# Kernel tuning notes

Measured on AMD Instinct MI355X. Metric: run time of the kernel, lower is better.

## Reference

```python
import jax, jax.numpy as jnp
import numpy as np

B, T, H, HEADS, K, L = 64, 512, 512, 4, 3, 16
R, A = 256, 9


def _pe(t, h):
    pos = np.arange(t)[:, None].astype(np.float32)
    div = np.exp(-np.log(10000.0) * np.arange(0, h, 2).astype(np.float32) / h)
    pe = np.zeros((t, h), np.float32)
    pe[:, 0::2] = np.sin(pos * div)
    pe[:, 1::2] = np.cos(pos * div)
    return jnp.asarray(pe)


def _ln(x, g, b, eps=1e-5):
    m = x.mean(-1, keepdims=True)
    v = ((x - m) ** 2).mean(-1, keepdims=True)
    return (x - m) * jax.lax.rsqrt(v + eps) * g + b


def _dwconv(x, k):
    # x [B,T,C], k [K,C]: depthwise temporal conv, SAME padding
    kern = k[:, None, :]  # [K, 1, C] in WIO layout, groups = C
    return jax.lax.conv_general_dilated(
        x, kern, (1,), 'SAME',
        dimension_numbers=('NWC', 'WIO', 'NWC'),
        feature_group_count=x.shape[-1])


def setup_inputs():
    key = jax.random.key(0)
    ks = jax.random.split(key, 16)
    n = lambda i, shape, s=0.02: jax.random.normal(ks[i], shape, jnp.float32) * s
    return dict(
        rssi=jax.random.normal(ks[0], (B, T, R), jnp.float32),
        accl=jax.random.normal(ks[1], (B, T, A), jnp.float32),
        rssi_W=n(2, (R, H)), rssi_b=jnp.zeros((H,), jnp.float32),
        accl_W=n(3, (A, H)), accl_b=jnp.zeros((H,), jnp.float32),
        conv_r=n(4, (K, H), 0.1), conv_a=n(5, (K, H), 0.1),
        Wq=n(6, (H, H)), Wk=n(7, (H, H)), Wv=n(8, (H, H)), Wo=n(9, (H, H)),
        ln1_g=jnp.ones((H,), jnp.float32), ln1_b=jnp.zeros((H,), jnp.float32),
        W1=n(10, (H, 4 * H)), b1=jnp.zeros((4 * H,), jnp.float32),
        W2=n(11, (4 * H, H)), b2=jnp.zeros((H,), jnp.float32),
        ln2_g=jnp.ones((H,), jnp.float32), ln2_b=jnp.zeros((H,), jnp.float32),
        loc_W=n(12, (H, L)), loc_b=jnp.zeros((L,), jnp.float32),
        start_trans=n(13, (L,), 0.1), end_trans=n(14, (L,), 0.1),
        trans=n(15, (L, L), 0.1),
    )


def _emissions(rssi, accl, rssi_W, rssi_b, accl_W, accl_b, conv_r, conv_a,
               Wq, Wk, Wv, Wo, ln1_g, ln1_b, W1, b1, W2, b2, ln2_g, ln2_b,
               loc_W, loc_b):
    t, h = rssi.shape[1], rssi_W.shape[1]
    pe = _pe(t, h)
    r = rssi @ rssi_W + rssi_b + pe                   # [B,T,H]
    a = accl @ accl_W + accl_b + pe                   # [B,T,H]
    x = _dwconv(r, conv_r) + _dwconv(a, conv_a)       # dual-conv fusion
    b_, t_, _ = x.shape
    dh = h // HEADS
    q = (x @ Wq).reshape(b_, t_, HEADS, dh)
    k = (x @ Wk).reshape(b_, t_, HEADS, dh)
    v = (x @ Wv).reshape(b_, t_, HEADS, dh)
    logits = jnp.einsum('bqhd,bkhd->bhqk', q, k) / jnp.sqrt(jnp.float32(dh))
    attn = jax.nn.softmax(logits, axis=-1)
    o = jnp.einsum('bhqk,bkhd->bqhd', attn, v).reshape(b_, t_, h) @ Wo
    x = _ln(x + o, ln1_g, ln1_b)
    f = jax.nn.relu(x @ W1 + b1) @ W2 + b2
    x = _ln(x + f, ln2_g, ln2_b)
    return x @ loc_W + loc_b                          # emissions [B,T,L]


def _viterbi(em, start_trans, end_trans, trans):
    # torchcrf-style Viterbi decode (batch_first, full-length sequences)
    score0 = start_trans + em[:, 0]                   # [B,L]

    def step(score, em_t):
        tot = score[:, :, None] + trans[None] + em_t[:, None, :]  # [B,L,L]
        return tot.max(axis=1), tot.argmax(axis=1)

    score, hist = jax.lax.scan(step, score0, jnp.swapaxes(em[:, 1:], 0, 1))
    final = score + end_trans
    last = jnp.argmax(final, axis=-1)                 # [B]
    best = jnp.max(final, axis=-1)                    # [B] best-path score

    def back(tag, h):
        prev = jnp.take_along_axis(h, tag[:, None], axis=1)[:, 0]
        return prev, prev

    _, path = jax.lax.scan(back, last, hist, reverse=True)
    tags = jnp.concatenate([path, last[None]], axis=0)  # [T,B]
    return jnp.swapaxes(tags, 0, 1).astype(jnp.int64), best


def reference(rssi, accl, rssi_W, rssi_b, accl_W, accl_b, conv_r, conv_a,
              Wq, Wk, Wv, Wo, ln1_g, ln1_b, W1, b1, W2, b2, ln2_g, ln2_b,
              loc_W, loc_b, start_trans, end_trans, trans):
    em = _emissions(rssi, accl, rssi_W, rssi_b, accl_W, accl_b, conv_r, conv_a,
                    Wq, Wk, Wv, Wo, ln1_g, ln1_b, W1, b1, W2, b2,
                    ln2_g, ln2_b, loc_W, loc_b)
    tags, _ = _viterbi(em, start_trans, end_trans, trans)
    return tags  # [B,T] int decoded locations
```

## Files before the change

kernel.cpp:

```cpp
#include <hip/hip_runtime.h>
#include <math.h>

constexpr int Bc = 64, Tc = 512, Hc = 512, HEADSc = 4, Lc = 16, Rc = 256, Ac = 9;
constexpr int DH = 128;

#define F_BIAS 1
#define F_PE   2
#define F_ADDC 4
#define F_RELU 8
#define F_DIV  16
#define F_QKV  32

using short8   = __attribute__((ext_vector_type(8)))  short;
using floatx16 = __attribute__((ext_vector_type(16))) float;
using ushort4v = __attribute__((ext_vector_type(4)))  unsigned short;

struct S3 { unsigned short h, m, l; };
__device__ inline S3 split3(float v)
{
    S3 r;
    unsigned u = __float_as_uint(v);
    r.h = (unsigned short)(u >> 16);
    float r1 = v - __uint_as_float(u & 0xffff0000u);
    unsigned u1 = __float_as_uint(r1);
    r.m = (unsigned short)(u1 >> 16);
    float r2 = r1 - __uint_as_float(u1 & 0xffff0000u);
    r.l = (unsigned short)(__float_as_uint(r2) >> 16);
    return r;
}

template<bool ASP, bool BSP>
__global__ __launch_bounds__(256)
void mgemm(const float* __restrict__ Af, const unsigned short* __restrict__ Asp,
           long long aPS,
           const float* __restrict__ Bf, const unsigned short* __restrict__ Bsp,
           long long bPS,
           float* __restrict__ C, const float* __restrict__ bias,
           const float* __restrict__ pe,
           int M, int N, int K, int lda, int ldb, int ldc,
           long long s1A, long long s2A, long long s1B, long long s2B,
           long long s1C, long long s2C, float divv, int flags)
{
    int z = blockIdx.z, z1 = z >> 2, z2 = z & 3;
    if (ASP) Asp += (size_t)z1 * s1A + (size_t)z2 * s2A;
    else     Af  += (size_t)z1 * s1A + (size_t)z2 * s2A;
    if (BSP) Bsp += (size_t)z1 * s1B + (size_t)z2 * s2B;
    else     Bf  += (size_t)z1 * s1B + (size_t)z2 * s2B;
    if (!(flags & F_QKV)) C += (size_t)z1 * s1C + (size_t)z2 * s2C;

    __shared__ unsigned short As[3][128][34];
    __shared__ unsigned short Bs[3][128][34];

    int bm = blockIdx.y * 128, bn = blockIdx.x * 128;
    int tid = threadIdx.x;
    int lane = tid & 63, wave = tid >> 6;
    int wr = wave >> 1, wc = wave & 1;
    int l31 = lane & 31, khalf = lane >> 5;

    floatx16 acc[2][2];
    #pragma unroll
    for (int i = 0; i < 2; i++)
        #pragma unroll
        for (int j = 0; j < 2; j++)
            #pragma unroll
            for (int e = 0; e < 16; e++) acc[i][j][e] = 0.f;

    for (int k0 = 0; k0 < K; k0 += 32) {
        if (ASP) {
            #pragma unroll
            for (int it = 0; it < 2; it++) {
                int s = tid + 256 * it;
                int rr = s >> 2, kc = (s & 3) << 3;
                size_t ga = (size_t)(bm + rr) * lda + k0 + kc;
                *(short8*)&As[0][rr][kc] = *(const short8*)(Asp + ga);
                *(short8*)&As[1][rr][kc] = *(const short8*)(Asp + aPS + ga);
                *(short8*)&As[2][rr][kc] = *(const short8*)(Asp + 2 * aPS + ga);
            }
        } else {
            #pragma unroll
            for (int it = 0; it < 4; it++) {
                int s = tid + 256 * it;
                int mm = s >> 3, kc = (s & 7) << 2;
                float4 v = *(const float4*)(Af + (size_t)(bm + mm) * lda + k0 + kc);
                ushort4v h, m, l;
                S3 s0 = split3(v.x); h[0] = s0.h; m[0] = s0.m; l[0] = s0.l;
                S3 s1 = split3(v.y); h[1] = s1.h; m[1] = s1.m; l[1] = s1.l;
                S3 s2 = split3(v.z); h[2] = s2.h; m[2] = s2.m; l[2] = s2.l;
                S3 s3 = split3(v.w); h[3] = s3.h; m[3] = s3.m; l[3] = s3.l;
                *(ushort4v*)&As[0][mm][kc] = h;
                *(ushort4v*)&As[1][mm][kc] = m;
                *(ushort4v*)&As[2][mm][kc] = l;
            }
        }
        if (BSP) {
            #pragma unroll
            for (int it = 0; it < 2; it++) {
                int s = tid + 256 * it;
                int nn = s >> 2, kc = (s & 3) << 3;
                size_t gb = (size_t)(bn + nn) * ldb + k0 + kc;
                *(short8*)&Bs[0][nn][kc] = *(const short8*)(Bsp + gb);
                *(short8*)&Bs[1][nn][kc] = *(const short8*)(Bsp + bPS + gb);
                *(short8*)&Bs[2][nn][kc] = *(const short8*)(Bsp + 2 * bPS + gb);
            }
        } else {
            #pragma unroll
            for (int it = 0; it < 4; it++) {
                int s = tid + 256 * it;
                int nn = s >> 3, kc = (s & 7) << 2;
                float4 v = *(const float4*)(Bf + (size_t)(bn + nn) * ldb + k0 + kc);
                ushort4v h, m, l;
                S3 s0 = split3(v.x); h[0] = s0.h; m[0] = s0.m; l[0] = s0.l;
                S3 s1 = split3(v.y); h[1] = s1.h; m[1] = s1.m; l[1] = s1.l;
                S3 s2 = split3(v.z); h[2] = s2.h; m[2] = s2.m; l[2] = s2.l;
                S3 s3 = split3(v.w); h[3] = s3.h; m[3] = s3.m; l[3] = s3.l;
                *(ushort4v*)&Bs[0][nn][kc] = h;
                *(ushort4v*)&Bs[1][nn][kc] = m;
                *(ushort4v*)&Bs[2][nn][kc] = l;
            }
        }
        __syncthreads();

        #pragma unroll
        for (int s = 0; s < 2; s++) {
            int ko = s * 16 + khalf * 8;
            short8 a0[2], a1[2], a2[2], b0[2], b1[2], b2[2];
            #pragma unroll
            for (int i = 0; i < 2; i++) {
                int ar = wr * 64 + i * 32 + l31;
                a0[i] = *(const short8*)&As[0][ar][ko];
                a1[i] = *(const short8*)&As[1][ar][ko];
                a2[i] = *(const short8*)&As[2][ar][ko];
                int br = wc * 64 + i * 32 + l31;
                b0[i] = *(const short8*)&Bs[0][br][ko];
                b1[i] = *(const short8*)&Bs[1][br][ko];
                b2[i] = *(const short8*)&Bs[2][br][ko];
            }
            #pragma unroll
            for (int i = 0; i < 2; i++)
                #pragma unroll
                for (int j = 0; j < 2; j++)
                    acc[i][j] = __builtin_amdgcn_mfma_f32_32x32x16_bf16(a0[i], b0[j], acc[i][j], 0, 0, 0);
            #pragma unroll
            for (int i = 0; i < 2; i++)
                #pragma unroll
                for (int j = 0; j < 2; j++)
                    acc[i][j] = __builtin_amdgcn_mfma_f32_32x32x16_bf16(a0[i], b1[j], acc[i][j], 0, 0, 0);
            #pragma unroll
            for (int i = 0; i < 2; i++)
                #pragma unroll
                for (int j = 0; j < 2; j++)
                    acc[i][j] = __builtin_amdgcn_mfma_f32_32x32x16_bf16(a1[i], b0[j], acc[i][j], 0, 0, 0);
            #pragma unroll
            for (int i = 0; i < 2; i++)
                #pragma unroll
                for (int j = 0; j < 2; j++)
                    acc[i][j] = __builtin_amdgcn_mfma_f32_32x32x16_bf16(a0[i], b2[j], acc[i][j], 0, 0, 0);
            #pragma unroll
            for (int i = 0; i < 2; i++)
                #pragma unroll
                for (int j = 0; j < 2; j++)
                    acc[i][j] = __builtin_amdgcn_mfma_f32_32x32x16_bf16(a2[i], b0[j], acc[i][j], 0, 0, 0);
            #pragma unroll
            for (int i = 0; i < 2; i++)
                #pragma unroll
                for (int j = 0; j < 2; j++)
                    acc[i][j] = __builtin_amdgcn_mfma_f32_32x32x16_bf16(a1[i], b1[j], acc[i][j], 0, 0, 0);
        }
        __syncthreads();
    }

    #pragma unroll
    for (int i = 0; i < 2; i++) {
        #pragma unroll
        for (int j = 0; j < 2; j++) {
            #pragma unroll
            for (int r = 0; r < 16; r++) {
                int m = bm + wr * 64 + i * 32 + (r & 3) + ((r >> 2) << 3) + (khalf << 2);
                int n = bn + wc * 64 + j * 32 + l31;
                float v = acc[i][j][r];
                if (flags & F_DIV)  v /= divv;
                if (flags & F_BIAS) v += bias[n];
                if (flags & F_PE)   v += pe[(size_t)(m & (Tc - 1)) * Hc + n];
                if (flags & F_QKV) {
                    long long gth = s1C;
                    if (n < 512) {
                        C[(size_t)m * 512 + n] = v;
                    } else if (n < 1024) {
                        C[gth + (size_t)m * 512 + (n - 512)] = v;
                    } else {
                        C[2 * gth + (size_t)(m >> 9) * (Tc * Hc)
                          + (size_t)(n - 1024) * Tc + (m & (Tc - 1))] = v;
                    }
                } else {
                    if (flags & F_ADDC) v += C[(size_t)m * ldc + n];
                    if (flags & F_RELU) v = fmaxf(v, 0.f);
                    C[(size_t)m * ldc + n] = v;
                }
            }
        }
    }
}

__global__ __launch_bounds__(256)
void asplit_kernel(const float* __restrict__ X, unsigned short* __restrict__ out,
                   long long PS, long long E)
{
    long long off = ((long long)blockIdx.x * 256 + threadIdx.x) * 8;
    if (off >= E) return;
    float4 v0 = *(const float4*)(X + off);
    float4 v1 = *(const float4*)(X + off + 4);
    short8 h, m, l;
    float vv[8] = {v0.x, v0.y, v0.z, v0.w, v1.x, v1.y, v1.z, v1.w};
    #pragma unroll
    for (int i = 0; i < 8; i++) {
        S3 s = split3(vv[i]);
        h[i] = (short)s.h; m[i] = (short)s.m; l[i] = (short)s.l;
    }
    *(short8*)(out + off) = h;
    *(short8*)(out + PS + off) = m;
    *(short8*)(out + 2 * PS + off) = l;
}

__global__ __launch_bounds__(256)
void wsplit_kernel(const float* __restrict__ W, unsigned short* __restrict__ out,
                   int K, int N, long long PS)
{
    __shared__ float t[64][65];
    int k0 = blockIdx.x * 64, n0 = blockIdx.y * 64;
    int tid = threadIdx.x;
    int c = tid & 63, r4 = tid >> 6;
    #pragma unroll
    for (int i = 0; i < 16; i++) {
        int r = r4 * 16 + i;
        t[r][c] = W[(size_t)(k0 + r) * N + n0 + c];
    }
    __syncthreads();
    #pragma unroll
    for (int i = 0; i < 16; i++) {
        int n = r4 * 16 + i;
        S3 s = split3(t[c][n]);
        size_t o = (size_t)(n0 + n) * K + k0 + c;
        out[o] = s.h; out[PS + o] = s.m; out[2 * PS + o] = s.l;
    }
}

__global__ void pe_kernel(float* __restrict__ pe)
{
    int idx = blockIdx.x * 256 + threadIdx.x;
    if (idx >= Tc * Hc) return;
    int t = idx >> 9, n = idx & (Hc - 1);
    int j = n >> 1;
    double div = exp(-log(10000.0) * (double)(2 * j) / (double)Hc);
    double arg = (double)t * div;
    pe[idx] = (float)((n & 1) ? cos(arg) : sin(arg));
}

__global__ __launch_bounds__(256)
void dwconv_fused_kernel(const float* __restrict__ r,
                         const float* __restrict__ accl,
                         const float* __restrict__ aW, const float* __restrict__ ab,
                         const float* __restrict__ pe,
                         const float* __restrict__ cr, const float* __restrict__ ca,
                         float* __restrict__ x)
{
    int idx = blockIdx.x * 256 + threadIdx.x;
    int c = idx & (Hc - 1);
    int m = idx >> 9;
    int t = m & (Tc - 1);
    float w[Ac];
    #pragma unroll
    for (int i = 0; i < Ac; i++) w[i] = aW[i * Hc + c];
    float bb = ab[c];

    auto aval = [&](int mm, int tt) {
        const float* row = accl + (size_t)mm * Ac;
        float s = 0.f;
        #pragma unroll
        for (int i = 0; i < Ac; i++) s += row[i] * w[i];
        return s + bb + pe[tt * Hc + c];
    };

    float vr = r[idx] * cr[Hc + c];
    float va = aval(m, t) * ca[Hc + c];
    if (t > 0) {
        vr = r[idx - Hc] * cr[c] + vr;
        va = aval(m - 1, t - 1) * ca[c] + va;
    }
    if (t < Tc - 1) {
        vr = vr + r[idx + Hc] * cr[2 * Hc + c];
        va = va + aval(m + 1, t + 1) * ca[2 * Hc + c];
    }
    x[idx] = vr + va;
}

__global__ __launch_bounds__(256)
void softmax_kernel(float* __restrict__ L)
{
    size_t base = (size_t)blockIdx.x * 512;
    int tid = threadIdx.x;
    float v0 = L[base + tid], v1 = L[base + tid + 256];
    __shared__ float buf[256];
    buf[tid] = fmaxf(v0, v1);
    __syncthreads();
    for (int s = 128; s > 0; s >>= 1) {
        if (tid < s) buf[tid] = fmaxf(buf[tid], buf[tid + s]);
        __syncthreads();
    }
    float mx = buf[0];
    __syncthreads();
    float e0 = expf(v0 - mx), e1 = expf(v1 - mx);
    buf[tid] = e0 + e1;
    __syncthreads();
    for (int s = 128; s > 0; s >>= 1) {
        if (tid < s) buf[tid] += buf[tid + s];
        __syncthreads();
    }
    float sum = buf[0];
    L[base + tid] = e0 / sum;
    L[base + tid + 256] = e1 / sum;
}

__global__ __launch_bounds__(256)
void add_ln_kernel(const float* __restrict__ X, const float* __restrict__ Y,
                   const float* __restrict__ g, const float* __restrict__ bta,
                   float* __restrict__ out)
{
    size_t base = (size_t)blockIdx.x * 512;
    int tid = threadIdx.x;
    float v0 = X[base + tid] + Y[base + tid];
    float v1 = X[base + tid + 256] + Y[base + tid + 256];
    __shared__ float buf[256];
    buf[tid] = v0 + v1;
    __syncthreads();
    for (int s = 128; s > 0; s >>= 1) {
        if (tid < s) buf[tid] += buf[tid + s];
        __syncthreads();
    }
    float mean = buf[0] / 512.f;
    __syncthreads();
    float d0 = v0 - mean, d1 = v1 - mean;
    buf[tid] = d0 * d0 + d1 * d1;
    __syncthreads();
    for (int s = 128; s > 0; s >>= 1) {
        if (tid < s) buf[tid] += buf[tid + s];
        __syncthreads();
    }
    float var = buf[0] / 512.f;
    float rs = 1.0f / sqrtf(var + 1e-5f);
    out[base + tid]       = d0 * rs * g[tid] + bta[tid];
    out[base + tid + 256] = d1 * rs * g[tid + 256] + bta[tid + 256];
}

__global__ __launch_bounds__(256)
void em_kernel(const float* __restrict__ X, const float* __restrict__ W,
               const float* __restrict__ bias, float* __restrict__ out)
{
    __shared__ float Wl[8192];
    int tid = threadIdx.x;
    #pragma unroll
    for (int i = 0; i < 32; i++) Wl[tid + 256 * i] = W[tid + 256 * i];
    __syncthreads();
    int r = tid >> 4, l = tid & 15;
    const float* xr = X + ((size_t)blockIdx.x * 16 + r) * Hc;
    float s = 0.f;
    #pragma unroll 8
    for (int k = 0; k < Hc; k++) s += xr[k] * Wl[k * Lc + l];
    s += bias[l];
    out[((size_t)blockIdx.x * 16 + r) * Lc + l] = s;
}

__device__ inline unsigned long long vit_pack(float v, int idx)
{
    unsigned u = __float_as_uint(v);
    unsigned ou = (u & 0x80000000u) ? ~u : (u | 0x80000000u);
    return ((unsigned long long)ou << 8) | (unsigned)idx;
}
__device__ inline float vit_unpack(unsigned long long p)
{
    unsigned ou = (unsigned)(p >> 8);
    unsigned u = (ou & 0x80000000u) ? (ou & 0x7fffffffu) : ~ou;
    return __uint_as_float(u);
}

__global__ __launch_bounds__(64)
void viterbi_kernel(const float* __restrict__ em, const float* __restrict__ st,
                    const float* __restrict__ et, const float* __restrict__ trans,
                    int* __restrict__ out)
{
    int b = blockIdx.x;
    int tid = threadIdx.x;
    int j = tid & 15, q = tid >> 4;
    __shared__ float ems[2][64][Lc];
    __shared__ unsigned char hist[Tc - 1][Lc];
    float tr0 = trans[(4 * q + 0) * Lc + j];
    float tr1 = trans[(4 * q + 1) * Lc + j];
    float tr2 = trans[(4 * q + 2) * Lc + j];
    float tr3 = trans[(4 * q + 3) * Lc + j];
    const float* emb = em + (size_t)b * Tc * Lc;
    {
        const float4* src = (const float4*)emb;
        float4* dst = (float4*)&ems[0][0][0];
        #pragma unroll
        for (int i = 0; i < 4; i++) dst[tid + 64 * i] = src[tid + 64 * i];
    }
    __syncthreads();
    float sc = st[j] + ems[0][0][j];
    for (int c = 0; c < 8; c++) {
        if (c < 7) {
            const float4* src = (const float4*)(emb + (size_t)(c + 1) * 64 * Lc);
            float4* dst = (float4*)&ems[(c + 1) & 1][0][0];
            #pragma unroll
            for (int i = 0; i < 4; i++) dst[tid + 64 * i] = src[tid + 64 * i];
        }
        int tt0 = (c == 0) ? 1 : 0;
        for (int tt = tt0; tt < 64; tt++) {
            int t = c * 64 + tt;
            float e = ems[c & 1][tt][j];
            float s0 = __shfl(sc, 4 * q + 0);
            float s1 = __shfl(sc, 4 * q + 1);
            float s2 = __shfl(sc, 4 * q + 2);
            float s3 = __shfl(sc, 4 * q + 3);
            unsigned long long p = vit_pack((s0 + tr0) + e, 15 - (4 * q + 0));
            unsigned long long p1 = vit_pack((s1 + tr1) + e, 15 - (4 * q + 1));
            unsigned long long p2 = vit_pack((s2 + tr2) + e, 15 - (4 * q + 2));
            unsigned long long p3 = vit_pack((s3 + tr3) + e, 15 - (4 * q + 3));
            if (p1 > p) p = p1;
            if (p2 > p) p = p2;
            if (p3 > p) p = p3;
            unsigned long long po = __shfl_xor(p, 16);
            if (po > p) p = po;
            po = __shfl_xor(p, 32);
            if (po > p) p = po;
            sc = vit_unpack(p);
            if (q == 0) hist[t - 1][j] = (unsigned char)(15 - (int)(p & 0xFF));
        }
        __syncthreads();
    }
    float fv = sc + et[j];
    float bv = __shfl(fv, 0);
    int tag = 0;
    #pragma unroll
    for (int i = 1; i < Lc; i++) {
        float v = __shfl(fv, i);
        if (v > bv) { bv = v; tag = i; }
    }
    __syncthreads();
    if (tid == 0) {
        out[(size_t)b * Tc + (Tc - 1)] = tag;
        for (int t = Tc - 2; t >= 0; t--) {
            tag = hist[t][tag];
            out[(size_t)b * Tc + t] = tag;
        }
    }
}

__global__ void diag_kernel(int* __restrict__ out, int n, int val)
{
    int i = blockIdx.x * 256 + threadIdx.x;
    if (i < n) out[i] = val;
}

extern "C" void kernel_launch(void* const* d_in, const int* in_sizes, int n_in,
                              void* d_out, int out_size, void* d_ws, size_t ws_size,
                              hipStream_t stream)
{
    const float* rssi   = (const float*)d_in[0];
    const float* accl   = (const float*)d_in[1];
    const float* rssi_W = (const float*)d_in[2];
    const float* rssi_b = (const float*)d_in[3];
    const float* accl_W = (const float*)d_in[4];
    const float* accl_b = (const float*)d_in[5];
    const float* conv_r = (const float*)d_in[6];
    const float* conv_a = (const float*)d_in[7];
    const float* Wq     = (const float*)d_in[8];
    const float* Wk     = (const float*)d_in[9];
    const float* Wv     = (const float*)d_in[10];
    const float* Wo     = (const float*)d_in[11];
    const float* ln1_g  = (const float*)d_in[12];
    const float* ln1_b  = (const float*)d_in[13];
    const float* W1     = (const float*)d_in[14];
    const float* b1     = (const float*)d_in[15];
    const float* W2     = (const float*)d_in[16];
    const float* b2     = (const float*)d_in[17];
    const float* ln2_g  = (const float*)d_in[18];
    const float* ln2_b  = (const float*)d_in[19];
    const float* loc_W  = (const float*)d_in[20];
    const float* loc_b  = (const float*)d_in[21];
    const float* start_trans = (const float*)d_in[22];
    const float* end_trans   = (const float*)d_in[23];
    const float* trans       = (const float*)d_in[24];

    const int M = Bc * Tc;
    const size_t S = (size_t)M * Hc;
    const size_t TH = (size_t)Tc * Hc;
    const long long TT = (long long)Tc * Tc;
    const float sq = sqrtf((float)DH);
    dim3 blk(256);

    const size_t WBUF_SH = 9830400ull;
    const size_t WBUF_F  = WBUF_SH / 2;
    size_t total_f = ws_size / sizeof(float);
    if (total_f < 2 * S + WBUF_F + TH + (size_t)M * 128) {
        diag_kernel<<<dim3((out_size + 255) / 256), blk, 0, stream>>>(
            (int*)d_out, out_size, 1000000 + (int)(ws_size >> 20));
        return;
    }

    float* bufX = (float*)d_ws;
    float* bufY = bufX + S;
    unsigned short* wbuf  = (unsigned short*)(bufY + S);
    unsigned short* rssiT = wbuf;
    unsigned short* qkvT  = wbuf + 393216;
    unsigned short* WoT   = wbuf + 2752512;
    unsigned short* W1T   = wbuf + 3538944;
    unsigned short* W2T   = wbuf + 6684672;
    float* pe_buf = (float*)(wbuf + WBUF_SH);
    float* work = pe_buf + TH;
    size_t work_n = total_f - 2 * S - WBUF_F - TH;

    int Ge = 1;
    for (int g = 64; g >= 1; g >>= 1) if ((size_t)g * TH <= work_n) { Ge = g; break; }
    int Ga = 1;
    for (int g = 64; g >= 1; g >>= 1)
        if ((19ull * g * TH) / 2 <= work_n) { Ga = g; break; }
    const size_t X1S_F = 25165824ull;
    bool ASP1 = (work_n >= X1S_F + (size_t)M * 128);
    int Nc = 128;
    {
        size_t base = ASP1 ? X1S_F : 0;
        for (int n = 2048; n >= 128; n >>= 1)
            if (base + (size_t)M * n <= work_n) { Nc = n; break; }
    }

    pe_kernel<<<dim3((Tc * Hc + 255) / 256), blk, 0, stream>>>(pe_buf);
    wsplit_kernel<<<dim3(Rc / 64, Hc / 64), blk, 0, stream>>>(rssi_W, rssiT, Rc, Hc, 131072LL);
    wsplit_kernel<<<dim3(8, 8),  blk, 0, stream>>>(Wq, qkvT,          512, 512, 786432LL);
    wsplit_kernel<<<dim3(8, 8),  blk, 0, stream>>>(Wk, qkvT + 262144, 512, 512, 786432LL);
    wsplit_kernel<<<dim3(8, 8),  blk, 0, stream>>>(Wv, qkvT + 524288, 512, 512, 786432LL);
    wsplit_kernel<<<dim3(8, 8),  blk, 0, stream>>>(Wo, WoT, 512, 512, 262144LL);
    wsplit_kernel<<<dim3(8, 32), blk, 0, stream>>>(W1, W1T, 512, 2048, 1048576LL);
    wsplit_kernel<<<dim3(32, 8), blk, 0, stream>>>(W2, W2T, 2048, 512, 1048576LL);

    for (int g0 = 0; g0 < Bc; g0 += Ge) {
        int rows = Ge * Tc;
        mgemm<false, true><<<dim3(Hc / 128, rows / 128, 1), blk, 0, stream>>>(
            rssi + (size_t)g0 * Tc * Rc, nullptr, 0,
            nullptr, rssiT, 131072LL,
            work, rssi_b, pe_buf,
            rows, Hc, Rc, Rc, Rc, Hc,
            0, 0, 0, 0, 0, 0, 1.f, F_BIAS | F_PE);
        dwconv_fused_kernel<<<dim3(rows * (Hc / 256)), blk, 0, stream>>>(
            work, accl + (size_t)g0 * Tc * Ac, accl_W, accl_b, pe_buf,
            conv_r, conv_a, bufX + (size_t)g0 * TH);
    }

    for (int g0 = 0; g0 < Bc; g0 += Ga) {
        int g = Ga;
        int rows = g * Tc;
        long long gth = (long long)g * TH;
        float* qg = work;
        float* kg = work + gth;
        float* vT = work + 2 * gth;
        float* og = work + 3 * gth;
        float* lg = work + 4 * gth;
        unsigned short* xsS = (unsigned short*)(work + 8 * gth);
        asplit_kernel<<<dim3((unsigned)(gth / 2048)), blk, 0, stream>>>(
            bufX + (size_t)g0 * TH, xsS, gth, gth);
        mgemm<true, true><<<dim3(12, rows / 128, 1), blk, 0, stream>>>(
            nullptr, xsS, gth,
            nullptr, qkvT, 786432LL,
            qg, nullptr, nullptr,
            rows, 1536, Hc, Hc, 512, 0,
            0, 0, 0, 0, gth, 0, 1.f, F_QKV);
        mgemm<false, false><<<dim3(Tc / 128, Tc / 128, g * HEADSc), blk, 0, stream>>>(
            qg, nullptr, 0, kg, nullptr, 0,
            lg, nullptr, nullptr,
            Tc, Tc, DH, Hc, Hc, Tc,
            (long long)TH, DH, (long long)TH, DH,
            (long long)HEADSc * TT, TT, sq, F_DIV);
        softmax_kernel<<<dim3(g * HEADSc * Tc), blk, 0, stream>>>(lg);
        mgemm<false, false><<<dim3(1, Tc / 128, g * HEADSc), blk, 0, stream>>>(
            lg, nullptr, 0, vT, nullptr, 0,
            og, nullptr, nullptr,
            Tc, DH, Tc, Tc, Tc, Hc,
            (long long)HEADSc * TT, TT,
            (long long)TH, (long long)DH * Tc,
            (long long)TH, DH, 1.f, 0);
        mgemm<false, true><<<dim3(Hc / 128, rows / 128, 1), blk, 0, stream>>>(
            og, nullptr, 0, nullptr, WoT, 262144LL,
            bufY + (size_t)g0 * TH, nullptr, nullptr,
            rows, Hc, Hc, Hc, 512, Hc,
            0, 0, 0, 0, 0, 0, 1.f, 0);
    }

    add_ln_kernel<<<dim3(M), blk, 0, stream>>>(bufX, bufY, ln1_g, ln1_b, bufX);

    unsigned short* x1S = (unsigned short*)work;
    float* hbuf = work + (ASP1 ? X1S_F : 0);
    if (ASP1) {
        asplit_kernel<<<dim3(M * 512 / 2048), blk, 0, stream>>>(
            bufX, x1S, (long long)M * 512, (long long)M * 512);
    }
    int nChunks = 2048 / Nc;
    for (int c = 0; c < nChunks; c++) {
        if (ASP1) {
            mgemm<true, true><<<dim3(Nc / 128, M / 128, 1), blk, 0, stream>>>(
                nullptr, x1S, (long long)M * 512,
                nullptr, W1T + (size_t)c * Nc * 512, 1048576LL,
                hbuf, b1 + c * Nc, nullptr,
                M, Nc, Hc, Hc, 512, Nc,
                0, 0, 0, 0, 0, 0, 1.f, F_BIAS | F_RELU);
        } else {
            mgemm<false, true><<<dim3(Nc / 128, M / 128, 1), blk, 0, stream>>>(
                bufX, nullptr, 0,
                nullptr, W1T + (size_t)c * Nc * 512, 1048576LL,
                hbuf, b1 + c * Nc, nullptr,
                M, Nc, Hc, Hc, 512, Nc,
                0, 0, 0, 0, 0, 0, 1.f, F_BIAS | F_RELU);
        }
        mgemm<false, true><<<dim3(Hc / 128, M / 128, 1), blk, 0, stream>>>(
            hbuf, nullptr, 0,
            nullptr, W2T + (size_t)c * Nc, 1048576LL,
            bufY, b2, nullptr,
            M, Hc, Nc, Nc, 2048, Hc,
            0, 0, 0, 0, 0, 0, 1.f, (c == 0) ? F_BIAS : F_ADDC);
    }

    add_ln_kernel<<<dim3(M), blk, 0, stream>>>(bufX, bufY, ln2_g, ln2_b, bufX);

    em_kernel<<<dim3(M / 16), blk, 0, stream>>>(bufX, loc_W, loc_b, work);

    viterbi_kernel<<<dim3(Bc), dim3(64), 0, stream>>>(
        work, start_trans, end_trans, trans, (int*)d_out);
}
```

Before: 3.221 ms.

## Chunk FFN over row groups instead of hidden columns; pad LDS rows

The FFN is restructured to process groups of rows at a time. Each group's activations are pre-split once, then the full 2048-wide hidden layer and the W2 projection run without F_ADDC accumulation passes over the output. Before, the FFN was split by hidden-dimension columns, which needed repeated read-modify-write of the output buffer and multiple kernel launches. LDS tile rows are also padded from 34 to 40 shorts, which changes the bank-conflict pattern and alignment at the cost of extra shared memory per block.

```diff
diff --git a/kernel.cpp b/kernel.cpp
--- a/kernel.cpp
+++ b/kernel.cpp
@@ -48,8 +48,8 @@
     else     Bf  += (size_t)z1 * s1B + (size_t)z2 * s2B;
     if (!(flags & F_QKV)) C += (size_t)z1 * s1C + (size_t)z2 * s2C;
 
-    __shared__ unsigned short As[3][128][34];
-    __shared__ unsigned short Bs[3][128][34];
+    __shared__ unsigned short As[3][128][40];
+    __shared__ unsigned short Bs[3][128][40];
 
     int bm = blockIdx.y * 128, bn = blockIdx.x * 128;
     int tid = threadIdx.x;
@@ -523,14 +523,6 @@
     int Ga = 1;
     for (int g = 64; g >= 1; g >>= 1)
         if ((19ull * g * TH) / 2 <= work_n) { Ga = g; break; }
-    const size_t X1S_F = 25165824ull;
-    bool ASP1 = (work_n >= X1S_F + (size_t)M * 128);
-    int Nc = 128;
-    {
-        size_t base = ASP1 ? X1S_F : 0;
-        for (int n = 2048; n >= 128; n >>= 1)
-            if (base + (size_t)M * n <= work_n) { Nc = n; break; }
-    }
 
     pe_kernel<<<dim3((Tc * Hc + 255) / 256), blk, 0, stream>>>(pe_buf);
     wsplit_kernel<<<dim3(Rc / 64, Hc / 64), blk, 0, stream>>>(rssi_W, rssiT, Rc, Hc, 131072LL);
@@ -595,35 +587,49 @@
 
     add_ln_kernel<<<dim3(M), blk, 0, stream>>>(bufX, bufY, ln1_g, ln1_b, bufX);
 
-    unsigned short* x1S = (unsigned short*)work;
-    float* hbuf = work + (ASP1 ? X1S_F : 0);
-    if (ASP1) {
-        asplit_kernel<<<dim3(M * 512 / 2048), blk, 0, stream>>>(
-            bufX, x1S, (long long)M * 512, (long long)M * 512);
-    }
-    int nChunks = 2048 / Nc;
-    for (int c = 0; c < nChunks; c++) {
-        if (ASP1) {
-            mgemm<true, true><<<dim3(Nc / 128, M / 128, 1), blk, 0, stream>>>(
-                nullptr, x1S, (long long)M * 512,
-                nullptr, W1T + (size_t)c * Nc * 512, 1048576LL,
-                hbuf, b1 + c * Nc, nullptr,
-                M, Nc, Hc, Hc, 512, Nc,
+    int Mg = 0;
+    for (int mg = 32768; mg >= 4096; mg >>= 1)
+        if ((size_t)mg * 2816 <= work_n) { Mg = mg; break; }
+    if (Mg) {
+        for (int mg0 = 0; mg0 < M; mg0 += Mg) {
+            unsigned short* x1S = (unsigned short*)work;
+            long long x1PS = (long long)Mg * 512;
+            float* hbuf = work + (size_t)Mg * 768;
+            asplit_kernel<<<dim3((unsigned)(x1PS / 2048)), blk, 0, stream>>>(
+                bufX + (size_t)mg0 * 512, x1S, x1PS, x1PS);
+            mgemm<true, true><<<dim3(16, Mg / 128, 1), blk, 0, stream>>>(
+                nullptr, x1S, x1PS,
+                nullptr, W1T, 1048576LL,
+                hbuf, b1, nullptr,
+                Mg, 2048, Hc, Hc, 512, 2048,
                 0, 0, 0, 0, 0, 0, 1.f, F_BIAS | F_RELU);
-        } else {
+            mgemm<false, true><<<dim3(4, Mg / 128, 1), blk, 0, stream>>>(
+                hbuf, nullptr, 0,
+                nullptr, W2T, 1048576LL,
+                bufY + (size_t)mg0 * 512, b2, nullptr,
+                Mg, Hc, 2048, 2048, 2048, Hc,
+                0, 0, 0, 0, 0, 0, 1.f, F_BIAS);
+        }
+    } else {
+        int Nc = 128;
+        for (int n = 2048; n >= 128; n >>= 1)
+            if ((size_t)M * n <= work_n) { Nc = n; break; }
+        float* hbuf = work;
+        int nChunks = 2048 / Nc;
+        for (int c = 0; c < nChunks; c++) {
             mgemm<false, true><<<dim3(Nc / 128, M / 128, 1), blk, 0, stream>>>(
                 bufX, nullptr, 0,
                 nullptr, W1T + (size_t)c * Nc * 512, 1048576LL,
                 hbuf, b1 + c * Nc, nullptr,
                 M, Nc, Hc, Hc, 512, Nc,
                 0, 0, 0, 0, 0, 0, 1.f, F_BIAS | F_RELU);
-        }
-        mgemm<false, true><<<dim3(Hc / 128, M / 128, 1), blk, 0, stream>>>(
-            hbuf, nullptr, 0,
-            nullptr, W2T + (size_t)c * Nc, 1048576LL,
-            bufY, b2, nullptr,
-            M, Hc, Nc, Nc, 2048, Hc,
-            0, 0, 0, 0, 0, 0, 1.f, (c == 0) ? F_BIAS : F_ADDC);
+            mgemm<false, true><<<dim3(Hc / 128, M / 128, 1), blk, 0, stream>>>(
+                hbuf, nullptr, 0,
+                nullptr, W2T + (size_t)c * Nc, 1048576LL,
+                bufY, b2, nullptr,
+                M, Hc, Nc, Nc, 2048, Hc,
+                0, 0, 0, 0, 0, 0, 1.f, (c == 0) ? F_BIAS : F_ADDC);
+        }
     }
 
     add_ln_kernel<<<dim3(M), blk, 0, stream>>>(bufX, bufY, ln2_g, ln2_b, bufX);
```

After: 3.734 ms. +15.9%, slower.
